# Kernel optimization log

Hardware: AMD Instinct MI355X
Metric: run time of the kernel (lower is better)

Reference implementation:

```python
import jax, jax.numpy as jnp
import numpy as np

N = 200000   # nodes
D = 256      # input_dim == output_dim
E = 6400000  # nnz per adjacency (avg degree 32)


def setup_inputs() -> dict:
    key = jax.random.key(0)
    ks = jax.random.split(key, 10)
    return {
        "x": jax.random.normal(ks[0], (N, D), dtype=jnp.float32),
        "w0": jax.random.normal(ks[1], (D, D), dtype=jnp.float32) * (1.0 / np.sqrt(D)),
        "w1": jax.random.normal(ks[2], (D, D), dtype=jnp.float32) * (1.0 / np.sqrt(D)),
        "bias": jax.random.normal(ks[3], (D,), dtype=jnp.float32) * 0.01,
        "vals0": jax.random.uniform(ks[4], (E,), dtype=jnp.float32),
        "vals1": jax.random.uniform(ks[5], (E,), dtype=jnp.float32),
        "rows0": jax.random.randint(ks[6], (E,), 0, N, dtype=jnp.int32),
        "cols0": jax.random.randint(ks[7], (E,), 0, N, dtype=jnp.int32),
        "rows1": jax.random.randint(ks[8], (E,), 0, N, dtype=jnp.int32),
        "cols1": jax.random.randint(ks[9], (E,), 0, N, dtype=jnp.int32),
    }


def _spmm(rows, cols, vals, dense, n):
    # sparse [n,n] @ dense [n,d] via gather + segment-sum scatter
    msg = vals[:, None] * dense[cols]          # [E, d]
    return jax.ops.segment_sum(msg, rows, num_segments=n)


def reference(x, w0, w1, bias, vals0, vals1, rows0, cols0, rows1, cols1):
    n = x.shape[0]
    # per-adjacency: dense projection then SpMM aggregation; sum over adjacencies
    h0 = _spmm(rows0, cols0, vals0, x @ w0, n)
    h1 = _spmm(rows1, cols1, vals1, x @ w1, n)
    return jnp.tanh(h0 + h1 + bias)
```

## Files before the change

### kernel.cpp

```cpp
#include <hip/hip_runtime.h>
#include <cstdint>

#define N_NODES 200000
#define DIM 256
#define NNZ 6400000

#define NB 782
#define BUCKET_CAP 17408
#define CHUNK 4096

using f16 = _Float16;
typedef __attribute__((ext_vector_type(8))) _Float16 f16x8;
typedef __attribute__((ext_vector_type(4))) float f32x4;

__global__ __launch_bounds__(256) void x16_kernel(const float* __restrict__ x,
                                                  f16* __restrict__ x16) {
    long i = (long)blockIdx.x * 256 + threadIdx.x;
    const f32x4* xv = reinterpret_cast<const f32x4*>(x);
    f32x4 v0 = xv[i * 2];
    f32x4 v1 = xv[i * 2 + 1];
    f16x8 h;
    h[0] = (f16)v0[0]; h[1] = (f16)v0[1]; h[2] = (f16)v0[2]; h[3] = (f16)v0[3];
    h[4] = (f16)v1[0]; h[5] = (f16)v1[1]; h[6] = (f16)v1[2]; h[7] = (f16)v1[3];
    reinterpret_cast<f16x8*>(x16)[i] = h;
}

__global__ void init_cursor(int* __restrict__ cursor) {
    int i = blockIdx.x * 256 + threadIdx.x;
    if (i < NB) cursor[i] = i * BUCKET_CAP;
}

__global__ __launch_bounds__(256) void bucket_scatter(
    const int* __restrict__ rows0, const int* __restrict__ cols0, const float* __restrict__ vals0,
    const int* __restrict__ rows1, const int* __restrict__ cols1, const float* __restrict__ vals1,
    int* __restrict__ bucket_cursor, unsigned long long* __restrict__ tmp) {
    __shared__ int hist[NB];
    __shared__ int base[NB];
    const int t = threadIdx.x;
    const long e0 = (long)blockIdx.x * CHUNK;

    int er[16];
    unsigned ec[16];
    float ev[16];
#pragma unroll
    for (int k = 0; k < 16; k++) {
        long e = e0 + t + k * 256;
        if (e < NNZ) {
            er[k] = rows0[e];
            ec[k] = (unsigned)cols0[e] * 2u;
            ev[k] = vals0[e];
        } else {
            long e1 = e - NNZ;
            er[k] = rows1[e1];
            ec[k] = (unsigned)cols1[e1] * 2u + 1u;
            ev[k] = vals1[e1];
        }
    }

    for (int i = t; i < NB; i += 256) hist[i] = 0;
    __syncthreads();

#pragma unroll
    for (int k = 0; k < 16; k++) atomicAdd(&hist[er[k] >> 8], 1);
    __syncthreads();

    for (int i = t; i < NB; i += 256) {
        int c = hist[i];
        base[i] = c ? atomicAdd(&bucket_cursor[i], c) : 0;
        hist[i] = 0;
    }
    __syncthreads();

#pragma unroll
    for (int k = 0; k < 16; k++) {
        int r = er[k];
        int b = r >> 8;
        int pos = base[b] + atomicAdd(&hist[b], 1);
        if (pos < (b + 1) * BUCKET_CAP) {
            unsigned col = ec[k] >> 1, adj = ec[k] & 1u;
            unsigned fine = (unsigned)(r & 255) * 2u + adj;
            unsigned lo = col | (fine << 18);
            tmp[pos] = (unsigned long long)lo | ((unsigned long long)__float_as_uint(ev[k]) << 32);
        }
    }
}

__global__ void bucket_scan(const int* __restrict__ bucket_cursor, int* __restrict__ bucket_base) {
    __shared__ int cnt[NB + 1];
    int t = threadIdx.x;
    for (int i = t; i < NB; i += 256) {
        int c = bucket_cursor[i] - i * BUCKET_CAP;
        cnt[i] = (c > BUCKET_CAP) ? BUCKET_CAP : c;
    }
    __syncthreads();
    if (t == 0) {
        int run = 0;
        for (int i = 0; i < NB; i++) {
            int c = cnt[i];
            cnt[i] = run;
            run += c;
        }
        cnt[NB] = run;
    }
    __syncthreads();
    for (int i = t; i <= NB; i += 256) bucket_base[i] = cnt[i];
}

__global__ __launch_bounds__(256) void bucket_sort(
    const unsigned long long* __restrict__ tmp, const int* __restrict__ bucket_cursor,
    const int* __restrict__ bucket_base, unsigned* __restrict__ colval,
    int* __restrict__ row_start2) {
    __shared__ int hist[512];
    __shared__ int offs[512];
    __shared__ int psc[256];
    const int b = blockIdx.x;
    const int t = threadIdx.x;
    int cnt = bucket_cursor[b] - b * BUCKET_CAP;
    if (cnt > BUCKET_CAP) cnt = BUCKET_CAP;
    const int gbase = bucket_base[b];
    const long tbase = (long)b * BUCKET_CAP;

    hist[t] = 0;
    hist[t + 256] = 0;
    __syncthreads();
    for (int i = t; i < cnt; i += 256) {
        unsigned lo = (unsigned)tmp[tbase + i];
        atomicAdd(&hist[(lo >> 18) & 511], 1);
    }
    __syncthreads();

    int s0 = hist[2 * t], s1 = hist[2 * t + 1];
    int s = s0 + s1;
    psc[t] = s;
    __syncthreads();
    for (int off = 1; off < 256; off <<= 1) {
        int v = (t >= off) ? psc[t - off] : 0;
        __syncthreads();
        psc[t] += v;
        __syncthreads();
    }
    int excl = psc[t] - s;
    offs[2 * t] = excl;
    offs[2 * t + 1] = excl + s0;

    int rowg = b * 256 + t;
    if (rowg < N_NODES) {
        row_start2[2 * rowg] = gbase + excl;
        row_start2[2 * rowg + 1] = gbase + excl + s0;
    }
    if (b == 0 && t == 0) row_start2[2 * N_NODES] = bucket_base[NB];
    hist[t] = 0;
    hist[t + 256] = 0;
    __syncthreads();

    for (int i = t; i < cnt; i += 256) {
        unsigned long long v = tmp[tbase + i];
        unsigned lo = (unsigned)v;
        int bin = (lo >> 18) & 511;
        float val = __uint_as_float((unsigned)(v >> 32));
        unsigned q = (unsigned)(val * 16383.f + 0.5f);
        unsigned rec = (lo & 0x3FFFFu) | (q << 18);
        int pos = gbase + offs[bin] + atomicAdd(&hist[bin], 1);
        colval[pos] = rec;
    }
}

__global__ void wpack_kernel(const float* __restrict__ w0, const float* __restrict__ w1,
                             f16* __restrict__ bpack) {
    int idx = blockIdx.x * 256 + threadIdx.x;
    int lane = idx & 63;
    int ct = (idx >> 6) & 31;
    int kstep = idx >> 11;
    int col = ct * 16 + (lane & 15);
    int k0 = kstep * 32 + (lane >> 4) * 8;
    const float* w = (col < 256) ? w0 : w1;
    int c = col & 255;
    union { f16 h[8]; uint4 u; } pk;
#pragma unroll
    for (int j = 0; j < 8; j++) pk.h[j] = (f16)w[(k0 + j) * 256 + c];
    reinterpret_cast<uint4*>(bpack)[idx] = pk.u;
}

__global__ __launch_bounds__(512) void fused_kernel(const f16* __restrict__ x16,
                                                    const unsigned* __restrict__ colval,
                                                    const int* __restrict__ row_start2,
                                                    const f16* __restrict__ bpack,
                                                    const float* __restrict__ bias,
                                                    float* __restrict__ out) {
    __shared__ uint4 xs[32 * 64];
    __shared__ unsigned se[8][64];
    __shared__ float sb[256];
    const int t = threadIdx.x;
    const int w = t >> 6, l = t & 63;
    const int h = l >> 5, s = l & 31;
    const long n0 = (long)blockIdx.x * 32;

    if (t < 256) sb[t] = bias[t];

    const char* xb = reinterpret_cast<const char*>(x16);
    const unsigned laneoff = (unsigned)s << 4;

    for (int it = 0; it < 8; ++it) {
        const int vl = w * 8 + it;
        const int nl = vl >> 1, adj = vl & 1;
        const long vrow = n0 * 2 + vl;
        int beg = row_start2[vrow];
        const int end = row_start2[vrow + 1];
        float acc[8] = {0.f, 0.f, 0.f, 0.f, 0.f, 0.f, 0.f, 0.f};

        while (beg < end) {
            int chunk = min(64, end - beg);
            if (l < chunk) se[w][l] = __builtin_nontemporal_load(&colval[beg + l]);
            __builtin_amdgcn_wave_barrier();
            int j = 0;
            for (; j + 16 <= chunk; j += 16) {
#pragma unroll
                for (int jj = 0; jj < 8; jj++) {
                    unsigned rec = se[w][j + jj * 2 + h];
                    float val = (float)(rec >> 18) * (1.f / 16383.f);
                    unsigned boff = ((rec & 0x3FFFFu) << 9) | laneoff;
                    f16x8 pv = *reinterpret_cast<const f16x8*>(xb + boff);
#pragma unroll
                    for (int k = 0; k < 8; k++) acc[k] = fmaf(val, (float)pv[k], acc[k]);
                }
            }
            for (; j < chunk; j += 2) {
                int e = j + h;
                unsigned rec = se[w][e < chunk ? e : j];
                float val = (e < chunk) ? (float)(rec >> 18) * (1.f / 16383.f) : 0.f;
                unsigned boff = ((rec & 0x3FFFFu) << 9) | laneoff;
                f16x8 pv = *reinterpret_cast<const f16x8*>(xb + boff);
#pragma unroll
                for (int k = 0; k < 8; k++) acc[k] = fmaf(val, (float)pv[k], acc[k]);
            }
            beg += chunk;
            __builtin_amdgcn_wave_barrier();
        }
#pragma unroll
        for (int k = 0; k < 8; k++) acc[k] += __shfl_xor(acc[k], 32);
        if (h == 0) {
            f16x8 r;
#pragma unroll
            for (int k = 0; k < 8; k++) r[k] = (f16)acc[k];
            reinterpret_cast<f16x8*>(xs)[nl * 64 + ((adj * 32 + s) ^ (nl & 7))] = r;
        }
    }
    __syncthreads();

    const int r = l & 15, q = l >> 4;
    const int ng = w & 1, ch = w >> 1;
    const int node = ng * 16 + r;
    const int swz = node & 7;

    f32x4 acc2[4];
#pragma unroll
    for (int c = 0; c < 4; c++) acc2[c] = (f32x4){0.f, 0.f, 0.f, 0.f};

    for (int kstep = 0; kstep < 8; kstep++) {
        f16x8 af0 = *reinterpret_cast<const f16x8*>(&xs[node * 64 + ((kstep * 4 + q) ^ swz)]);
        f16x8 af1 = *reinterpret_cast<const f16x8*>(&xs[node * 64 + ((32 + kstep * 4 + q) ^ swz)]);
        const f16x8* bp = reinterpret_cast<const f16x8*>(bpack) + (kstep * 32) * 64 + l;
#pragma unroll
        for (int c = 0; c < 4; c++) {
            int ct = ch * 4 + c;
            acc2[c] = __builtin_amdgcn_mfma_f32_16x16x32_f16(af0, bp[ct * 64], acc2[c], 0, 0, 0);
            acc2[c] =
                __builtin_amdgcn_mfma_f32_16x16x32_f16(af1, bp[(16 + ct) * 64], acc2[c], 0, 0, 0);
        }
    }

#pragma unroll
    for (int c = 0; c < 4; c++) {
        int col = (ch * 4 + c) * 16 + r;
        float b = sb[col];
#pragma unroll
        for (int i = 0; i < 4; i++) {
            long row = n0 + ng * 16 + q * 4 + i;
            out[row * 256 + col] = tanhf(acc2[c][i] + b);
        }
    }
}

extern "C" void kernel_launch(void* const* d_in, const int* in_sizes, int n_in,
                              void* d_out, int out_size, void* d_ws, size_t ws_size,
                              hipStream_t stream) {
    const float* x = (const float*)d_in[0];
    const float* w0 = (const float*)d_in[1];
    const float* w1 = (const float*)d_in[2];
    const float* bias = (const float*)d_in[3];
    const float* vals0 = (const float*)d_in[4];
    const float* vals1 = (const float*)d_in[5];
    const int* rows0 = (const int*)d_in[6];
    const int* cols0 = (const int*)d_in[7];
    const int* rows1 = (const int*)d_in[8];
    const int* cols1 = (const int*)d_in[9];
    float* out = (float*)d_out;

    char* ws = (char*)d_ws;
    size_t off = 0;
    auto alloc = [&](size_t bytes) -> void* {
        void* p = ws + off;
        off += (bytes + 255) & ~(size_t)255;
        return p;
    };
    f16* x16 = (f16*)alloc((size_t)N_NODES * DIM * sizeof(f16));
    unsigned* colval = (unsigned*)alloc((size_t)2 * NNZ * sizeof(unsigned));
    unsigned long long* tmp =
        (unsigned long long*)alloc((size_t)NB * BUCKET_CAP * sizeof(unsigned long long));
    int* row_start2 = (int*)alloc((size_t)(2 * N_NODES + 1) * sizeof(int));
    int* bucket_cursor = (int*)alloc((size_t)NB * sizeof(int));
    int* bucket_base = (int*)alloc((size_t)(NB + 1) * sizeof(int));
    f16* bpack = (f16*)alloc((size_t)2 * DIM * DIM * sizeof(f16));

    x16_kernel<<<25000, 256, 0, stream>>>(x, x16);

    init_cursor<<<(NB + 255) / 256, 256, 0, stream>>>(bucket_cursor);

    const long TOTAL_E = 2L * NNZ;
    const int nblkA = (int)(TOTAL_E / CHUNK);
    bucket_scatter<<<nblkA, 256, 0, stream>>>(rows0, cols0, vals0, rows1, cols1, vals1,
                                              bucket_cursor, tmp);

    bucket_scan<<<1, 256, 0, stream>>>(bucket_cursor, bucket_base);

    bucket_sort<<<NB, 256, 0, stream>>>(tmp, bucket_cursor, bucket_base, colval, row_start2);

    wpack_kernel<<<64, 256, 0, stream>>>(w0, w1, bpack);

    fused_kernel<<<N_NODES / 32, 512, 0, stream>>>(x16, colval, row_start2, bpack, bias, out);
}
```

Measured before the change: 1.288 ms.

## Merge prep kernels, widen bucket scatter/sort blocks, register-cache bucket entries

Folds the fp16 conversion of x, the weight packing and the cursor init into one prep launch, which removes two kernel launches. The bucket scatter now uses 1024-thread blocks over 16K-edge chunks with bounds guards, so fewer blocks contend on the global cursor atomics. Bucket sort uses 1024 threads and keeps each bucket's entries in registers, so tmp is read once instead of twice. It also switches to a 512-wide scan that writes row starts directly. The cost is higher register pressure, which may lower occupancy, and a longer scan with more barriers.

```diff
diff --git a/kernel.cpp b/kernel.cpp
--- a/kernel.cpp
+++ b/kernel.cpp
@@ -7,30 +7,49 @@
 
 #define NB 782
 #define BUCKET_CAP 17408
-#define CHUNK 4096
+#define CHUNK 16384
 
 using f16 = _Float16;
 typedef __attribute__((ext_vector_type(8))) _Float16 f16x8;
 typedef __attribute__((ext_vector_type(4))) float f32x4;
 
-__global__ __launch_bounds__(256) void x16_kernel(const float* __restrict__ x,
-                                                  f16* __restrict__ x16) {
-    long i = (long)blockIdx.x * 256 + threadIdx.x;
-    const f32x4* xv = reinterpret_cast<const f32x4*>(x);
-    f32x4 v0 = xv[i * 2];
-    f32x4 v1 = xv[i * 2 + 1];
-    f16x8 h;
-    h[0] = (f16)v0[0]; h[1] = (f16)v0[1]; h[2] = (f16)v0[2]; h[3] = (f16)v0[3];
-    h[4] = (f16)v1[0]; h[5] = (f16)v1[1]; h[6] = (f16)v1[2]; h[7] = (f16)v1[3];
-    reinterpret_cast<f16x8*>(x16)[i] = h;
-}
-
-__global__ void init_cursor(int* __restrict__ cursor) {
-    int i = blockIdx.x * 256 + threadIdx.x;
-    if (i < NB) cursor[i] = i * BUCKET_CAP;
-}
-
-__global__ __launch_bounds__(256) void bucket_scatter(
+__global__ __launch_bounds__(256) void prep_kernel(const float* __restrict__ x,
+                                                   f16* __restrict__ x16,
+                                                   const float* __restrict__ w0,
+                                                   const float* __restrict__ w1,
+                                                   f16* __restrict__ bpack,
+                                                   int* __restrict__ bucket_cursor) {
+    const int t = threadIdx.x;
+    const int bb = blockIdx.x;
+    if (bb < 25000) {
+        long i = (long)bb * 256 + t;
+        const f32x4* xv = reinterpret_cast<const f32x4*>(x);
+        f32x4 v0 = xv[i * 2];
+        f32x4 v1 = xv[i * 2 + 1];
+        f16x8 h;
+        h[0] = (f16)v0[0]; h[1] = (f16)v0[1]; h[2] = (f16)v0[2]; h[3] = (f16)v0[3];
+        h[4] = (f16)v1[0]; h[5] = (f16)v1[1]; h[6] = (f16)v1[2]; h[7] = (f16)v1[3];
+        reinterpret_cast<f16x8*>(x16)[i] = h;
+    } else if (bb < 25064) {
+        int idx = (bb - 25000) * 256 + t;
+        int lane = idx & 63;
+        int ct = (idx >> 6) & 31;
+        int kstep = idx >> 11;
+        int col = ct * 16 + (lane & 15);
+        int k0 = kstep * 32 + (lane >> 4) * 8;
+        const float* w = (col < 256) ? w0 : w1;
+        int c = col & 255;
+        union { f16 h[8]; uint4 u; } pk;
+#pragma unroll
+        for (int j = 0; j < 8; j++) pk.h[j] = (f16)w[(k0 + j) * 256 + c];
+        reinterpret_cast<uint4*>(bpack)[idx] = pk.u;
+    } else {
+        int i = (bb - 25064) * 256 + t;
+        if (i < NB) bucket_cursor[i] = i * BUCKET_CAP;
+    }
+}
+
+__global__ __launch_bounds__(1024) void bucket_scatter(
     const int* __restrict__ rows0, const int* __restrict__ cols0, const float* __restrict__ vals0,
     const int* __restrict__ rows1, const int* __restrict__ cols1, const float* __restrict__ vals1,
     int* __restrict__ bucket_cursor, unsigned long long* __restrict__ tmp) {
@@ -44,8 +63,12 @@
     float ev[16];
 #pragma unroll
     for (int k = 0; k < 16; k++) {
-        long e = e0 + t + k * 256;
-        if (e < NNZ) {
+        long e = e0 + t + k * 1024;
+        if (e >= 2L * NNZ) {
+            er[k] = -1;
+            ec[k] = 0u;
+            ev[k] = 0.f;
+        } else if (e < NNZ) {
             er[k] = rows0[e];
             ec[k] = (unsigned)cols0[e] * 2u;
             ev[k] = vals0[e];
@@ -57,14 +80,15 @@
         }
     }
 
-    for (int i = t; i < NB; i += 256) hist[i] = 0;
-    __syncthreads();
-
-#pragma unroll
-    for (int k = 0; k < 16; k++) atomicAdd(&hist[er[k] >> 8], 1);
-    __syncthreads();
-
-    for (int i = t; i < NB; i += 256) {
+    for (int i = t; i < NB; i += 1024) hist[i] = 0;
+    __syncthreads();
+
+#pragma unroll
+    for (int k = 0; k < 16; k++)
+        if (er[k] >= 0) atomicAdd(&hist[er[k] >> 8], 1);
+    __syncthreads();
+
+    for (int i = t; i < NB; i += 1024) {
         int c = hist[i];
         base[i] = c ? atomicAdd(&bucket_cursor[i], c) : 0;
         hist[i] = 0;
@@ -74,6 +98,7 @@
 #pragma unroll
     for (int k = 0; k < 16; k++) {
         int r = er[k];
+        if (r < 0) continue;
         int b = r >> 8;
         int pos = base[b] + atomicAdd(&hist[b], 1);
         if (pos < (b + 1) * BUCKET_CAP) {
@@ -106,13 +131,13 @@
     for (int i = t; i <= NB; i += 256) bucket_base[i] = cnt[i];
 }
 
-__global__ __launch_bounds__(256) void bucket_sort(
+__global__ __launch_bounds__(1024) void bucket_sort(
     const unsigned long long* __restrict__ tmp, const int* __restrict__ bucket_cursor,
     const int* __restrict__ bucket_base, unsigned* __restrict__ colval,
     int* __restrict__ row_start2) {
     __shared__ int hist[512];
+    __shared__ int psc[512];
     __shared__ int offs[512];
-    __shared__ int psc[256];
     const int b = blockIdx.x;
     const int t = threadIdx.x;
     int cnt = bucket_cursor[b] - b * BUCKET_CAP;
@@ -120,65 +145,57 @@
     const int gbase = bucket_base[b];
     const long tbase = (long)b * BUCKET_CAP;
 
-    hist[t] = 0;
-    hist[t + 256] = 0;
-    __syncthreads();
-    for (int i = t; i < cnt; i += 256) {
-        unsigned lo = (unsigned)tmp[tbase + i];
-        atomicAdd(&hist[(lo >> 18) & 511], 1);
-    }
-    __syncthreads();
-
-    int s0 = hist[2 * t], s1 = hist[2 * t + 1];
-    int s = s0 + s1;
-    psc[t] = s;
-    __syncthreads();
-    for (int off = 1; off < 256; off <<= 1) {
-        int v = (t >= off) ? psc[t - off] : 0;
+    unsigned long long rec[17];
+#pragma unroll
+    for (int k = 0; k < 17; k++) {
+        int i = t + k * 1024;
+        rec[k] = (i < cnt) ? tmp[tbase + i] : 0ULL;
+    }
+    if (t < 512) hist[t] = 0;
+    __syncthreads();
+
+#pragma unroll
+    for (int k = 0; k < 17; k++) {
+        int i = t + k * 1024;
+        if (i < cnt) {
+            unsigned lo = (unsigned)rec[k];
+            atomicAdd(&hist[(lo >> 18) & 511], 1);
+        }
+    }
+    __syncthreads();
+
+    if (t < 512) psc[t] = hist[t];
+    __syncthreads();
+    for (int off = 1; off < 512; off <<= 1) {
+        int v = (t < 512 && t >= off) ? psc[t - off] : 0;
         __syncthreads();
-        psc[t] += v;
+        if (t < 512) psc[t] += v;
         __syncthreads();
     }
-    int excl = psc[t] - s;
-    offs[2 * t] = excl;
-    offs[2 * t + 1] = excl + s0;
-
-    int rowg = b * 256 + t;
-    if (rowg < N_NODES) {
-        row_start2[2 * rowg] = gbase + excl;
-        row_start2[2 * rowg + 1] = gbase + excl + s0;
+    if (t < 512) {
+        int excl = psc[t] - hist[t];
+        offs[t] = excl;
+        long vrow = (long)b * 512 + t;
+        if (vrow < 2 * N_NODES) row_start2[vrow] = gbase + excl;
     }
     if (b == 0 && t == 0) row_start2[2 * N_NODES] = bucket_base[NB];
-    hist[t] = 0;
-    hist[t + 256] = 0;
-    __syncthreads();
-
-    for (int i = t; i < cnt; i += 256) {
-        unsigned long long v = tmp[tbase + i];
-        unsigned lo = (unsigned)v;
-        int bin = (lo >> 18) & 511;
-        float val = __uint_as_float((unsigned)(v >> 32));
-        unsigned q = (unsigned)(val * 16383.f + 0.5f);
-        unsigned rec = (lo & 0x3FFFFu) | (q << 18);
-        int pos = gbase + offs[bin] + atomicAdd(&hist[bin], 1);
-        colval[pos] = rec;
-    }
-}
-
-__global__ void wpack_kernel(const float* __restrict__ w0, const float* __restrict__ w1,
-                             f16* __restrict__ bpack) {
-    int idx = blockIdx.x * 256 + threadIdx.x;
-    int lane = idx & 63;
-    int ct = (idx >> 6) & 31;
-    int kstep = idx >> 11;
-    int col = ct * 16 + (lane & 15);
-    int k0 = kstep * 32 + (lane >> 4) * 8;
-    const float* w = (col < 256) ? w0 : w1;
-    int c = col & 255;
-    union { f16 h[8]; uint4 u; } pk;
-#pragma unroll
-    for (int j = 0; j < 8; j++) pk.h[j] = (f16)w[(k0 + j) * 256 + c];
-    reinterpret_cast<uint4*>(bpack)[idx] = pk.u;
+    __syncthreads();
+    if (t < 512) hist[t] = 0;
+    __syncthreads();
+
+#pragma unroll
+    for (int k = 0; k < 17; k++) {
+        int i = t + k * 1024;
+        if (i < cnt) {
+            unsigned lo = (unsigned)rec[k];
+            int bin = (lo >> 18) & 511;
+            float val = __uint_as_float((unsigned)(rec[k] >> 32));
+            unsigned q = (unsigned)(val * 16383.f + 0.5f);
+            unsigned orec = (lo & 0x3FFFFu) | (q << 18);
+            int pos = gbase + offs[bin] + atomicAdd(&hist[bin], 1);
+            colval[pos] = orec;
+        }
+    }
 }
 
 __global__ __launch_bounds__(512) void fused_kernel(const f16* __restrict__ x16,
@@ -312,20 +329,16 @@
     int* bucket_base = (int*)alloc((size_t)(NB + 1) * sizeof(int));
     f16* bpack = (f16*)alloc((size_t)2 * DIM * DIM * sizeof(f16));
 
-    x16_kernel<<<25000, 256, 0, stream>>>(x, x16);
-
-    init_cursor<<<(NB + 255) / 256, 256, 0, stream>>>(bucket_cursor);
+    prep_kernel<<<25068, 256, 0, stream>>>(x, x16, w0, w1, bpack, bucket_cursor);
 
     const long TOTAL_E = 2L * NNZ;
-    const int nblkA = (int)(TOTAL_E / CHUNK);
-    bucket_scatter<<<nblkA, 256, 0, stream>>>(rows0, cols0, vals0, rows1, cols1, vals1,
-                                              bucket_cursor, tmp);
+    const int nblkA = (int)((TOTAL_E + CHUNK - 1) / CHUNK);
+    bucket_scatter<<<nblkA, 1024, 0, stream>>>(rows0, cols0, vals0, rows1, cols1, vals1,
+                                               bucket_cursor, tmp);
 
     bucket_scan<<<1, 256, 0, stream>>>(bucket_cursor, bucket_base);
 
-    bucket_sort<<<NB, 256, 0, stream>>>(tmp, bucket_cursor, bucket_base, colval, row_start2);
-
-    wpack_kernel<<<64, 256, 0, stream>>>(w0, w1, bpack);
+    bucket_sort<<<NB, 1024, 0, stream>>>(tmp, bucket_cursor, bucket_base, colval, row_start2);
 
     fused_kernel<<<N_NODES / 32, 512, 0, stream>>>(x16, colval, row_start2, bpack, bias, out);
 }
```

After: 1.212 ms. 1.06x faster.
